# Kernel optimization log

Measured on AMD Instinct MI355X. Metric: run time of the kernel, lower is better.

## Reference

```python
import jax, jax.numpy as jnp
import numpy as np

N, E, G = 20000, 320000, 64
H, NF, EF, L, Z = 280, 5, 4, 3, 64
BN_EPS = 1e-5


def _bn(x, g, b):
    # BatchNorm1d in training mode: batch stats over dim 0, biased variance
    m = x.mean(0)
    v = x.var(0)
    return g * (x - m) * jax.lax.rsqrt(v + BN_EPS) + b


def _mlp(x, W1, b1, g1, be1, W2, b2, g2, be2):
    h = jax.nn.relu(_bn(x @ W1 + b1, g1, be1))
    return jax.nn.relu(_bn(h @ W2 + b2, g2, be2))


def setup_inputs() -> dict:
    key = jax.random.key(0)
    ks = jax.random.split(key, 24)
    s = 0.05
    inp = {
        "x": jax.random.normal(ks[0], (N, NF), jnp.float32),
        "edge_attr": jax.random.normal(ks[1], (E, EF), jnp.float32),
        "edge_index": jax.random.randint(ks[2], (2, E), 0, N),
        "batch": jnp.sort(jax.random.randint(ks[3], (N,), 0, G)),
        # input layer
        "Wi": jax.random.normal(ks[4], (NF, H), jnp.float32) * s,
        "bi": jnp.zeros((H,), jnp.float32),
        # message MLP (stacked over L layers): in = 2H+EF
        "Wm1": jax.random.normal(ks[5], (L, 2 * H + EF, H), jnp.float32) * s,
        "bm1": jnp.zeros((L, H), jnp.float32),
        "g1": jnp.ones((L, H), jnp.float32),
        "be1": jnp.zeros((L, H), jnp.float32),
        "Wm2": jax.random.normal(ks[6], (L, H, H), jnp.float32) * s,
        "bm2": jnp.zeros((L, H), jnp.float32),
        "g2": jnp.ones((L, H), jnp.float32),
        "be2": jnp.zeros((L, H), jnp.float32),
        # update MLP: in = 2H
        "Wu1": jax.random.normal(ks[7], (L, 2 * H, H), jnp.float32) * s,
        "bu1": jnp.zeros((L, H), jnp.float32),
        "g3": jnp.ones((L, H), jnp.float32),
        "be3": jnp.zeros((L, H), jnp.float32),
        "Wu2": jax.random.normal(ks[8], (L, H, H), jnp.float32) * s,
        "bu2": jnp.zeros((L, H), jnp.float32),
        "g4": jnp.ones((L, H), jnp.float32),
        "be4": jnp.zeros((L, H), jnp.float32),
        # mu head
        "Wmu": jax.random.normal(ks[9], (H, Z), jnp.float32) * s,
        "bmu": jnp.zeros((Z,), jnp.float32),
    }
    return inp


def reference(x, edge_attr, Wi, bi, Wm1, bm1, g1, be1, Wm2, bm2, g2, be2,
              Wu1, bu1, g3, be3, Wu2, bu2, g4, be4, Wmu, bmu,
              edge_index, batch):
    src, dst = edge_index[0], edge_index[1]
    h = x @ Wi + bi  # [N, H]
    for l in range(L):
        # message: cat(h_i=h[dst], h_j=h[src], edge_attr) -> MLP -> [E, H]
        msg_in = jnp.concatenate([h[dst], h[src], edge_attr], axis=-1)
        msg = _mlp(msg_in, Wm1[l], bm1[l], g1[l], be1[l], Wm2[l], bm2[l], g2[l], be2[l])
        # aggregate: scatter-add into target nodes
        agg = jax.ops.segment_sum(msg, dst, num_segments=N)
        # update: cat(h, agg) -> MLP; residual in GNNEncoder
        upd = _mlp(jnp.concatenate([h, agg], axis=-1),
                   Wu1[l], bu1[l], g3[l], be3[l], Wu2[l], bu2[l], g4[l], be4[l])
        h = h + upd
    # global mean pool over graphs
    sums = jax.ops.segment_sum(h, batch, num_segments=G)
    cnt = jax.ops.segment_sum(jnp.ones((h.shape[0],), h.dtype), batch, num_segments=G)
    pooled = sums / jnp.maximum(cnt, 1.0)[:, None]
    return pooled @ Wmu + bmu  # [G, Z]
```

## Files before the change

### kernel.cpp

```cpp
#include <hip/hip_runtime.h>
#include <hip/hip_bf16.h>

#define NN 20000
#define EE 320000
#define GG 64
#define HH 280
#define NFF 5
#define EFF 4
#define LL 3
#define ZZ 64
#define BN_EPS 1e-5f

typedef __hip_bfloat16 bf;
typedef unsigned short ush;
typedef __attribute__((ext_vector_type(8))) short v8s;
typedef __attribute__((ext_vector_type(4))) float v4f;

__device__ __forceinline__ float us2f(ush u) {
  return __uint_as_float(((unsigned)u) << 16);
}
__device__ __forceinline__ ush f2us(float v) {
  bf b = __float2bfloat16(v);
  return *reinterpret_cast<ush*>(&b);
}
__device__ __forceinline__ int clampi(int v, int hi) {
  return v < 0 ? 0 : (v >= hi ? hi - 1 : v);
}

__global__ void probe_k(const void* __restrict__ x, int* __restrict__ flag) {
  __shared__ int sh[256];
  int tid = threadIdx.x;
  int cnt = 0;
  for (int i = tid; i < 2048; i += 256) {
    ush w = ((const ush*)x)[i];
    unsigned e = (w >> 7) & 0xFF;
    if (w != 0 && (e < 87 || e > 167)) cnt++;
  }
  sh[tid] = cnt;
  __syncthreads();
  for (int o = 128; o > 0; o >>= 1) {
    if (tid < o) sh[tid] += sh[tid + o];
    __syncthreads();
  }
  if (tid == 0) *flag = (sh[0] > 64) ? 1 : 0;
}

__global__ void convert_k(const void* __restrict__ src, float* __restrict__ dst,
                          int n, const int* __restrict__ flag) {
  int i = blockIdx.x * 256 + threadIdx.x;
  if (i < n) {
    if (*flag)
      dst[i] = ((const float*)src)[i];
    else
      dst[i] = us2f(((const ush*)src)[i]);
  }
}

__global__ void wt_ab_k(const float* __restrict__ W, ush* __restrict__ O) {
  int i = blockIdx.x * 256 + threadIdx.x;
  if (i >= 3 * 576 * 288) return;
  int l = i / 165888, r = i % 165888;
  int n = r / 288, k = r % 288;
  float v = 0.f;
  if (n < 560 && k < 280)
    v = (n < 280) ? W[(size_t)l * 157920 + (size_t)k * 280 + n]
                  : W[(size_t)l * 157920 + (size_t)(280 + k) * 280 + (n - 280)];
  O[i] = f2us(v);
}
__global__ void wt_sq_k(const float* __restrict__ W, ush* __restrict__ O) {
  int i = blockIdx.x * 256 + threadIdx.x;
  if (i >= 3 * 320 * 288) return;
  int l = i / 92160, r = i % 92160;
  int n = r / 288, k = r % 288;
  float v = (n < 280 && k < 280) ? W[(size_t)l * 78400 + (size_t)k * 280 + n] : 0.f;
  O[i] = f2us(v);
}
__global__ void wt_u1_k(const float* __restrict__ W, ush* __restrict__ O) {
  int i = blockIdx.x * 256 + threadIdx.x;
  if (i >= 3 * 320 * 576) return;
  int l = i / 184320, r = i % 184320;
  int n = r / 576, k = r % 576;
  float v = (n < 280 && k < 560) ? W[(size_t)l * 156800 + (size_t)k * 280 + n] : 0.f;
  O[i] = f2us(v);
}

struct MG {
  const ush* A;
  const ush* Bt;
  const float* bias;
  void* C;
  float* stats;
  int M, K, Nn, lda, ldb, ldc;
};

template <int CB, int ST>
__global__ __launch_bounds__(256) void mgemm_k(MG g) {
  __shared__ ush As[64][40];
  __shared__ ush Bs[64][40];
  __shared__ float red[16][64];
  int t = threadIdx.x;
  int n0 = blockIdx.x * 64, m0 = blockIdx.y * 64;
  int lane = t & 63, wv = t >> 6;
  int lrow = lane & 15, quad = lane >> 4;
  int ar = t >> 2;
  int ac = (t & 3) << 3;
  v4f acc[4];
#pragma unroll
  for (int j = 0; j < 4; ++j) acc[j] = (v4f){0.f, 0.f, 0.f, 0.f};

  const ush* Ap = g.A + (size_t)(m0 + ar) * g.lda + ac;
  const ush* Bp = g.Bt + (size_t)(n0 + ar) * g.ldb + ac;
  bool av = (m0 + ar) < g.M;
  uint4 zz = {0, 0, 0, 0};

  int nkt = g.K >> 5;
  uint4 a0 = av ? *(const uint4*)Ap : zz;
  uint4 b0 = *(const uint4*)Bp;

  for (int kt = 0; kt < nkt; ++kt) {
    __syncthreads();
    *(uint4*)&As[ar][ac] = a0;
    *(uint4*)&Bs[ar][ac] = b0;
    __syncthreads();
    if (kt + 1 < nkt) {
      int kn = (kt + 1) << 5;
      a0 = av ? *(const uint4*)(Ap + kn) : zz;
      b0 = *(const uint4*)(Bp + kn);
    }
    v8s af = *(const v8s*)&As[(wv << 4) + lrow][quad << 3];
    v8s bq[4];
#pragma unroll
    for (int ci = 0; ci < 4; ++ci)
      bq[ci] = *(const v8s*)&Bs[(ci << 4) + lrow][quad << 3];
#pragma unroll
    for (int ci = 0; ci < 4; ++ci)
      acc[ci] = __builtin_amdgcn_mfma_f32_16x16x32_bf16(af, bq[ci], acc[ci],
                                                        0, 0, 0);
  }

  float bj[4];
#pragma unroll
  for (int ci = 0; ci < 4; ++ci) {
    int gn = n0 + (ci << 4) + lrow;
    bj[ci] = (g.bias && gn < g.Nn) ? g.bias[gn] : 0.f;
  }
#pragma unroll
  for (int ci = 0; ci < 4; ++ci)
#pragma unroll
    for (int r = 0; r < 4; ++r) {
      int gm = m0 + (wv << 4) + (quad << 2) + r;
      int gn = n0 + (ci << 4) + lrow;
      float v = acc[ci][r] + bj[ci];
      bool ok = (gm < g.M) && (gn < g.Nn);
      if (ok) {
        size_t idx = (size_t)gm * g.ldc + gn;
        if (CB)
          ((ush*)g.C)[idx] = f2us(v);
        else
          ((float*)g.C)[idx] = v;
      }
      acc[ci][r] = ok ? v : 0.f;
    }
  if (ST) {
    int rowg = (wv << 2) | quad;
#pragma unroll
    for (int ci = 0; ci < 4; ++ci) {
      float s = acc[ci][0] + acc[ci][1] + acc[ci][2] + acc[ci][3];
      red[rowg][(ci << 4) | lrow] = s;
    }
    __syncthreads();
    if (t < 64) {
      float s = 0.f;
#pragma unroll
      for (int r = 0; r < 16; ++r) s += red[r][t];
      int gn = n0 + t;
      if (gn < g.Nn) atomicAdd(&g.stats[gn], s);
    }
    __syncthreads();
#pragma unroll
    for (int ci = 0; ci < 4; ++ci) {
      float s = acc[ci][0] * acc[ci][0] + acc[ci][1] * acc[ci][1] +
                acc[ci][2] * acc[ci][2] + acc[ci][3] * acc[ci][3];
      red[rowg][(ci << 4) | lrow] = s;
    }
    __syncthreads();
    if (t < 64) {
      float s = 0.f;
#pragma unroll
      for (int r = 0; r < 16; ++r) s += red[r][t];
      int gn = n0 + t;
      if (gn < g.Nn) atomicAdd(&g.stats[HH + gn], s);
    }
  }
}

__global__ __launch_bounds__(256) void gemm_small_k(
    const float* __restrict__ A, const float* __restrict__ B,
    const float* __restrict__ bias, void* __restrict__ C,
    const int* __restrict__ flag, int M, int K, int Nn, int lda, int ldb,
    int ldc, int outmode) {
  __shared__ alignas(16) float As[16][68];
  __shared__ alignas(16) float Bsm[16][68];
  int tid = threadIdx.x;
  int n0 = blockIdx.x * 64, m0 = blockIdx.y * 64;
  int tx = tid & 15, ty = tid >> 4;
  int am = tid >> 2, akq = (tid & 3) << 2;
  int bk = tid >> 4, bn = (tid & 15) << 2;
  float acc[4][4] = {};
  int gmA = m0 + am;
  int nkt = (K + 15) >> 4;
  for (int kt = 0; kt < nkt; ++kt) {
    int k0 = kt << 4;
#pragma unroll
    for (int i = 0; i < 4; ++i) {
      int gk = k0 + akq + i;
      As[akq + i][am] = (gmA < M && gk < K) ? A[(size_t)gmA * lda + gk] : 0.f;
    }
    {
      int gk = k0 + bk;
      bool kin = gk < K;
#pragma unroll
      for (int j = 0; j < 4; ++j) {
        int gn = n0 + bn + j;
        Bsm[bk][bn + j] = (kin && gn < Nn) ? B[(size_t)gk * ldb + gn] : 0.f;
      }
    }
    __syncthreads();
#pragma unroll
    for (int kk = 0; kk < 16; ++kk) {
      float4 a4 = *(const float4*)&As[kk][ty << 2];
      float4 b4 = *(const float4*)&Bsm[kk][tx << 2];
      float av[4] = {a4.x, a4.y, a4.z, a4.w};
      float bv[4] = {b4.x, b4.y, b4.z, b4.w};
#pragma unroll
      for (int i = 0; i < 4; ++i)
#pragma unroll
        for (int j = 0; j < 4; ++j) acc[i][j] = fmaf(av[i], bv[j], acc[i][j]);
    }
    __syncthreads();
  }
  int ofl = outmode ? *flag : -1;
#pragma unroll
  for (int i = 0; i < 4; ++i) {
    int gm = m0 + (ty << 2) + i;
    if (gm < M) {
#pragma unroll
      for (int j = 0; j < 4; ++j) {
        int gn = n0 + (tx << 2) + j;
        if (gn < Nn) {
          float v = acc[i][j] + (bias ? bias[gn] : 0.f);
          size_t idx = (size_t)gm * ldc + gn;
          if (outmode == 0)
            ((float*)C)[idx] = v;
          else if (ofl)
            ((float*)C)[idx] = v;
          else
            ((ush*)C)[idx] = f2us(v);
        }
      }
    }
  }
}

__global__ __launch_bounds__(256) void edge_stats_k(
    const int* __restrict__ eids, const int* __restrict__ dst,
    const int* __restrict__ src, const float* __restrict__ ea,
    const ush* __restrict__ Pq, const float* __restrict__ W1c,
    const float* __restrict__ b1, float* __restrict__ stats) {
  __shared__ int dstl[256], srcl[256];
  __shared__ float4 eal[256];
  __shared__ float w1cs[4 * HH];
  __shared__ float b1s[HH];
  int tid = threadIdx.x;
  int e0 = blockIdx.x * 256;
  {
    int e = clampi(eids[e0 + tid], EE);
    dstl[tid] = clampi(dst[e], NN);
    srcl[tid] = clampi(src[e], NN);
    eal[tid] = *(const float4*)(ea + (size_t)e * 4);
  }
  for (int i = tid; i < 4 * HH; i += 256) w1cs[i] = W1c[i];
  for (int i = tid; i < HH; i += 256) b1s[i] = b1[i];
  __syncthreads();
  int c0 = tid, c1 = tid + 256;
  bool has1 = c1 < HH;
  float s0 = 0.f, q0 = 0.f, s1 = 0.f, q1 = 0.f;
  for (int e = 0; e < 256; ++e) {
    int d = dstl[e], sn = srcl[e];
    float4 ev = eal[e];
    {
      float raw = us2f(Pq[(size_t)d * 576 + c0]) + us2f(Pq[(size_t)sn * 576 + 280 + c0]);
      float r = ev.x * w1cs[c0] + ev.y * w1cs[HH + c0] +
                ev.z * w1cs[2 * HH + c0] + ev.w * w1cs[3 * HH + c0];
      float tv = raw + r + b1s[c0];
      s0 += tv; q0 += tv * tv;
    }
    if (has1) {
      float raw = us2f(Pq[(size_t)d * 576 + c1]) + us2f(Pq[(size_t)sn * 576 + 280 + c1]);
      float r = ev.x * w1cs[c1] + ev.y * w1cs[HH + c1] +
                ev.z * w1cs[2 * HH + c1] + ev.w * w1cs[3 * HH + c1];
      float tv = raw + r + b1s[c1];
      s1 += tv; q1 += tv * tv;
    }
  }
  atomicAdd(&stats[c0], s0);
  atomicAdd(&stats[HH + c0], q0);
  if (has1) {
    atomicAdd(&stats[c1], s1);
    atomicAdd(&stats[HH + c1], q1);
  }
}

__global__ void bn_finalize_k(const float* __restrict__ stats, float cnt,
                              const float* __restrict__ gw,
                              const float* __restrict__ bw,
                              const float* __restrict__ extra,
                              float* __restrict__ scale,
                              float* __restrict__ shift) {
  int c = threadIdx.x;
  if (c < HH) {
    float m = stats[c] / cnt;
    float v = stats[HH + c] / cnt - m * m;
    v = v < 0.f ? 0.f : v;
    float r = rsqrtf(v + BN_EPS);
    float sc = gw[c] * r;
    float sh = bw[c] - sc * m + (extra ? sc * extra[c] : 0.f);
    scale[c] = sc;
    shift[c] = sh;
  }
}

__global__ void hist_k(const int* __restrict__ dst, int* __restrict__ counts) {
  int e = blockIdx.x * 256 + threadIdx.x;
  if (e < EE) atomicAdd(&counts[clampi(dst[e], NN)], 1);
}

__global__ __launch_bounds__(1024) void scan_k(const int* __restrict__ counts,
                                               int* __restrict__ offs, int n) {
  __shared__ int buf[1024];
  __shared__ int running;
  int tid = threadIdx.x;
  if (tid == 0) running = 0;
  __syncthreads();
  for (int base = 0; base < n; base += 1024) {
    int v = (base + tid < n) ? counts[base + tid] : 0;
    buf[tid] = v;
    __syncthreads();
    for (int off = 1; off < 1024; off <<= 1) {
      int t = (tid >= off) ? buf[tid - off] : 0;
      __syncthreads();
      buf[tid] += t;
      __syncthreads();
    }
    int incl = buf[tid];
    if (base + tid < n) offs[base + tid] = running + incl - v;
    __syncthreads();
    if (tid == 1023) running += incl;
    __syncthreads();
  }
  if (tid == 0) offs[n] = running;
}

__global__ void fill_k(const int* __restrict__ dst, const int* __restrict__ offs,
                       int* __restrict__ cursor, int* __restrict__ eids) {
  int e = blockIdx.x * 256 + threadIdx.x;
  if (e < EE) {
    int n = clampi(dst[e], NN);
    int pos = atomicAdd(&cursor[n], 1);
    int idx = offs[n] + pos;
    if (idx >= 0 && idx < EE) eids[idx] = e;
  }
}

__global__ __launch_bounds__(256) void build_t1_k(
    const int* __restrict__ eids, const int* __restrict__ dst,
    const int* __restrict__ src, const float* __restrict__ ea,
    const ush* __restrict__ Pq, const float* __restrict__ W1c,
    const float* __restrict__ sc, const float* __restrict__ sh,
    ush* __restrict__ T1, int cb) {
  __shared__ float scs[HH], shs[HH], w1[4 * HH];
  int t = threadIdx.x;
  for (int i = t; i < HH; i += 256) { scs[i] = sc[i]; shs[i] = sh[i]; }
  for (int i = t; i < 4 * HH; i += 256) w1[i] = W1c[i];
  __syncthreads();
  int base = blockIdx.x * 32;
  int c2 = t + 256;
  bool h2 = c2 < HH;
  for (int i = 0; i < 32; ++i) {
    int r = cb + base + i;
    int e = clampi(eids[r], EE);
    int d = clampi(dst[e], NN), s = clampi(src[e], NN);
    float4 ev = *(const float4*)(ea + (size_t)e * 4);
    size_t pd = (size_t)d * 576, ps = (size_t)s * 576 + 280;
    size_t orow = (size_t)(base + i) * 288;
    {
      int c = t;
      float v = us2f(Pq[pd + c]) + us2f(Pq[ps + c]) + ev.x * w1[c] +
                ev.y * w1[HH + c] + ev.z * w1[2 * HH + c] + ev.w * w1[3 * HH + c];
      v = fmaf(scs[c], v, shs[c]);
      T1[orow + c] = f2us(v > 0.f ? v : 0.f);
    }
    if (h2) {
      int c = c2;
      float v = us2f(Pq[pd + c]) + us2f(Pq[ps + c]) + ev.x * w1[c] +
                ev.y * w1[HH + c] + ev.z * w1[2 * HH + c] + ev.w * w1[3 * HH + c];
      v = fmaf(scs[c], v, shs[c]);
      T1[orow + c] = f2us(v > 0.f ? v : 0.f);
    }
  }
}

__global__ __launch_bounds__(256) void aggregate_k(
    const int* __restrict__ offs, const ush* __restrict__ tmp2,
    const float* __restrict__ scale, const float* __restrict__ shift,
    float* __restrict__ agg, int e0, int e1) {
  int n = blockIdx.x;
  int rs = offs[n], re = offs[n + 1];
  if (rs < e0) rs = e0;
  if (re > e1) re = e1;
  if (rs >= re) return;
  int t = threadIdx.x;
  int c2 = t + 256;
  bool h2 = c2 < HH;
  float a0 = 0.f, a1 = 0.f;
  float sc0 = scale[t], sh0 = shift[t];
  float sc1 = h2 ? scale[c2] : 0.f, sh1 = h2 ? shift[c2] : 0.f;
  for (int r = rs; r < re; ++r) {
    const ush* row = tmp2 + (size_t)(r - e0) * HH;
    float v0 = fmaf(sc0, us2f(row[t]), sh0);
    a0 += v0 > 0.f ? v0 : 0.f;
    if (h2) {
      float v1 = fmaf(sc1, us2f(row[c2]), sh1);
      a1 += v1 > 0.f ? v1 : 0.f;
    }
  }
  agg[(size_t)n * HH + t] += a0;
  if (h2) agg[(size_t)n * HH + c2] += a1;
}

__global__ void hb_k(const float* __restrict__ h, ush* __restrict__ hcat) {
  int i = blockIdx.x * 256 + threadIdx.x;
  if (i < NN * HH) {
    int n = i / HH, c = i % HH;
    hcat[(size_t)n * 576 + c] = f2us(h[i]);
  }
}
__global__ void agg2hcat_k(const float* __restrict__ agg, ush* __restrict__ hcat) {
  int i = blockIdx.x * 256 + threadIdx.x;
  if (i < NN * HH) {
    int n = i / HH, c = i % HH;
    hcat[(size_t)n * 576 + 280 + c] = f2us(agg[i]);
  }
}
__global__ void u2a_k(const float* __restrict__ u1, const float* __restrict__ sc,
                      const float* __restrict__ sh, ush* __restrict__ u2A) {
  int i = blockIdx.x * 256 + threadIdx.x;
  if (i < NN * HH) {
    int n = i / HH, c = i % HH;
    float v = fmaf(sc[c], u1[i], sh[c]);
    u2A[(size_t)n * 288 + c] = f2us(v > 0.f ? v : 0.f);
  }
}
__global__ void residual_k(float* __restrict__ h, const float* __restrict__ u2,
                           const float* __restrict__ scale,
                           const float* __restrict__ shift) {
  int i = blockIdx.x * 256 + threadIdx.x;
  if (i < NN * HH) {
    int c = i % HH;
    float v = fmaf(scale[c], u2[i], shift[c]);
    h[i] += v > 0.f ? v : 0.f;
  }
}

__device__ __forceinline__ int lowerb(const int* a, int n, int key) {
  int lo = 0, hi = n;
  while (lo < hi) {
    int mid = (lo + hi) >> 1;
    if (a[mid] < key) lo = mid + 1; else hi = mid;
  }
  return lo;
}

__global__ __launch_bounds__(256) void pool_k(const float* __restrict__ h,
                                              const int* __restrict__ batch,
                                              float* __restrict__ pooled) {
  __shared__ float red[4][56];
  int gid = blockIdx.x, cc = blockIdx.y;
  int start = lowerb(batch, NN, gid);
  int end = lowerb(batch, NN, gid + 1);
  int cnt = end - start;
  float inv = 1.f / (float)(cnt > 1 ? cnt : 1);
  int grp = threadIdx.x >> 6, ci = threadIdx.x & 63;
  if (ci < 56) {
    int col = cc * 56 + ci;
    float s = 0.f;
    for (int n = start + grp; n < end; n += 4) s += h[(size_t)n * HH + col];
    red[grp][ci] = s;
  }
  __syncthreads();
  if (threadIdx.x < 56) {
    float s = red[0][threadIdx.x] + red[1][threadIdx.x] +
              red[2][threadIdx.x] + red[3][threadIdx.x];
    pooled[(size_t)gid * HH + cc * 56 + threadIdx.x] = s * inv;
  }
}

extern "C" void kernel_launch(void* const* d_in, const int* in_sizes, int n_in,
                              void* d_out, int out_size, void* d_ws,
                              size_t ws_size, hipStream_t stream) {
  const int* eidx = (const int*)d_in[2];
  const int* batch = (const int*)d_in[3];
  const int* srcp = eidx;
  const int* dstp = eidx + EE;
  size_t NH = (size_t)NN * HH;

  float* w0 = (float*)d_ws;
  size_t off = 0;
  auto alloc = [&](size_t n) {
    float* p = w0 + off;
    off += (n + 3) & ~(size_t)3;
    return p;
  };
  int* flag = (int*)alloc(4);
  float* cx = alloc(100000);
  float* cea = alloc(1280000);
  float* cWi = alloc(1400);
  float* cbi = alloc(280);
  float* cWm1 = alloc(473760);
  float* cbm1 = alloc(840);
  float* cg1 = alloc(840);
  float* cbe1 = alloc(840);
  float* cWm2 = alloc(235200);
  float* cbm2 = alloc(840);
  float* cg2 = alloc(840);
  float* cbe2 = alloc(840);
  float* cWu1 = alloc(470400);
  float* cbu1 = alloc(840);
  float* cg3 = alloc(840);
  float* cbe3 = alloc(840);
  float* cWu2 = alloc(235200);
  float* cbu2 = alloc(840);
  float* cg4 = alloc(840);
  float* cbe4 = alloc(840);
  float* cWmu = alloc(17920);
  float* cbmu = alloc(64);
  ush* W1ab = (ush*)alloc(248832);
  ush* W2t = (ush*)alloc(138240);
  ush* WU1t = (ush*)alloc(276480);
  ush* WU2t = (ush*)alloc(138240);
  float* h = alloc(NH);
  ush* hcat = (ush*)alloc(5824512);
  ush* u2A = hcat;
  float* pqr = alloc(5824512);
  ush* Pq = (ush*)pqr;
  float* u1f = pqr;
  float* agg = alloc(NH);
  float* pooled = alloc((size_t)GG * HH);
  float* stats = alloc(8 * HH);
  float* ss = alloc(8 * HH);
  int* counts = (int*)alloc(NN);
  int* offs = (int*)alloc(NN + 1);
  int* cursor = (int*)alloc(NN);
  int* eids = (int*)alloc(EE);
  size_t baseB = off * 4;

  int EC = 6400, T2 = 6400;
  {
    const int ecs[5] = {64000, 64000, 32000, 12800, 6400};
    const int t2s[5] = {EE, 64000, 32000, 12800, 6400};
    for (int i = 0; i < 5; ++i) {
      size_t need = baseB + (size_t)ecs[i] * 288 * 2 + (size_t)t2s[i] * 280 * 2 + 64;
      if (need <= ws_size) { EC = ecs[i]; T2 = t2s[i]; break; }
    }
  }
  ush* T1c = (ush*)(w0 + off);
  ush* tmp2 = T1c + (size_t)EC * 288;
  bool stored = (T2 == EE);
  int nch = EE / EC;

  probe_k<<<1, 256, 0, stream>>>(d_in[0], flag);
  struct Cv { const void* s; float* d; int n; };
  const Cv cv[22] = {
      {d_in[0], cx, NN * NFF},     {d_in[1], cea, EE * EFF},
      {d_in[4], cWi, NFF * HH},    {d_in[5], cbi, HH},
      {d_in[6], cWm1, LL * (2 * HH + EFF) * HH}, {d_in[7], cbm1, LL * HH},
      {d_in[8], cg1, LL * HH},     {d_in[9], cbe1, LL * HH},
      {d_in[10], cWm2, LL * HH * HH}, {d_in[11], cbm2, LL * HH},
      {d_in[12], cg2, LL * HH},    {d_in[13], cbe2, LL * HH},
      {d_in[14], cWu1, LL * 2 * HH * HH}, {d_in[15], cbu1, LL * HH},
      {d_in[16], cg3, LL * HH},    {d_in[17], cbe3, LL * HH},
      {d_in[18], cWu2, LL * HH * HH}, {d_in[19], cbu2, LL * HH},
      {d_in[20], cg4, LL * HH},    {d_in[21], cbe4, LL * HH},
      {d_in[22], cWmu, HH * ZZ},   {d_in[23], cbmu, ZZ}};
  for (int i = 0; i < 22; ++i)
    convert_k<<<(cv[i].n + 255) / 256, 256, 0, stream>>>(cv[i].s, cv[i].d, cv[i].n, flag);

  wt_ab_k<<<(3 * 576 * 288 + 255) / 256, 256, 0, stream>>>(cWm1, W1ab);
  wt_sq_k<<<(3 * 320 * 288 + 255) / 256, 256, 0, stream>>>(cWm2, W2t);
  wt_u1_k<<<(3 * 320 * 576 + 255) / 256, 256, 0, stream>>>(cWu1, WU1t);
  wt_sq_k<<<(3 * 320 * 288 + 255) / 256, 256, 0, stream>>>(cWu2, WU2t);

  gemm_small_k<<<dim3(5, 313), 256, 0, stream>>>(cx, cWi, cbi, h, nullptr, NN,
                                                 NFF, HH, NFF, HH, HH, 0);
  hipMemsetAsync(counts, 0, NN * sizeof(int), stream);
  hipMemsetAsync(cursor, 0, NN * sizeof(int), stream);
  hist_k<<<(EE + 255) / 256, 256, 0, stream>>>(dstp, counts);
  scan_k<<<1, 1024, 0, stream>>>(counts, offs, NN);
  fill_k<<<(EE + 255) / 256, 256, 0, stream>>>(dstp, offs, cursor, eids);

  int elemGrid = (int)((NH + 255) / 256);
  for (int l = 0; l < LL; ++l) {
    ush* Wab = W1ab + (size_t)l * 576 * 288;
    ush* W2l = W2t + (size_t)l * 320 * 288;
    ush* WU1l = WU1t + (size_t)l * 320 * 576;
    ush* WU2l = WU2t + (size_t)l * 320 * 288;
    const float* W1c = cWm1 + (size_t)l * 157920 + (size_t)560 * 280;
    float* st1 = stats; float* st2 = stats + 560;
    float* st3 = stats + 1120; float* st4 = stats + 1680;
    float* ss1 = ss; float* ss2 = ss + 560;
    float* ss3 = ss + 1120; float* ss4 = ss + 1680;
    hipMemsetAsync(stats, 0, 8 * HH * sizeof(float), stream);

    hb_k<<<elemGrid, 256, 0, stream>>>(h, hcat);
    {
      MG g = {hcat, Wab, nullptr, Pq, nullptr, NN, 288, 560, 576, 288, 576};
      mgemm_k<1, 0><<<dim3(9, 313), 256, 0, stream>>>(g);
    }
    edge_stats_k<<<EE / 256, 256, 0, stream>>>(eids, dstp, srcp, cea, Pq, W1c,
                                               cbm1 + l * HH, st1);
    bn_finalize_k<<<1, 320, 0, stream>>>(st1, (float)EE, cg1 + l * HH,
                                         cbe1 + l * HH, cbm1 + l * HH, ss1, ss1 + HH);
    for (int c = 0; c < nch; ++c) {
      int cb = c * EC;
      build_t1_k<<<EC / 32, 256, 0, stream>>>(eids, dstp, srcp, cea, Pq, W1c,
                                              ss1, ss1 + HH, T1c, cb);
      MG g = {T1c, W2l, cbm2 + l * HH,
              stored ? (void*)(tmp2 + (size_t)cb * HH) : (void*)tmp2, st2,
              EC, 288, HH, 288, 288, HH};
      mgemm_k<1, 1><<<dim3(5, EC / 64), 256, 0, stream>>>(g);
    }
    bn_finalize_k<<<1, 320, 0, stream>>>(st2, (float)EE, cg2 + l * HH,
                                         cbe2 + l * HH, nullptr, ss2, ss2 + HH);
    hipMemsetAsync(agg, 0, NH * sizeof(float), stream);
    if (stored) {
      aggregate_k<<<NN, 256, 0, stream>>>(offs, tmp2, ss2, ss2 + HH, agg, 0, EE);
    } else {
      for (int c = 0; c < nch; ++c) {
        int cb = c * EC;
        build_t1_k<<<EC / 32, 256, 0, stream>>>(eids, dstp, srcp, cea, Pq, W1c,
                                                ss1, ss1 + HH, T1c, cb);
        MG g = {T1c, W2l, cbm2 + l * HH, (void*)tmp2, nullptr,
                EC, 288, HH, 288, 288, HH};
        mgemm_k<1, 0><<<dim3(5, EC / 64), 256, 0, stream>>>(g);
        aggregate_k<<<NN, 256, 0, stream>>>(offs, tmp2, ss2, ss2 + HH, agg, cb, cb + EC);
      }
    }
    agg2hcat_k<<<elemGrid, 256, 0, stream>>>(agg, hcat);
    {
      MG g = {hcat, WU1l, cbu1 + l * HH, u1f, st3, NN, 576, HH, 576, 576, HH};
      mgemm_k<0, 1><<<dim3(5, 313), 256, 0, stream>>>(g);
    }
    bn_finalize_k<<<1, 320, 0, stream>>>(st3, (float)NN, cg3 + l * HH,
                                         cbe3 + l * HH, nullptr, ss3, ss3 + HH);
    u2a_k<<<elemGrid, 256, 0, stream>>>(u1f, ss3, ss3 + HH, u2A);
    {
      MG g = {u2A, WU2l, cbu2 + l * HH, agg, st4, NN, 288, HH, 288, 288, HH};
      mgemm_k<0, 1><<<dim3(5, 313), 256, 0, stream>>>(g);
    }
    bn_finalize_k<<<1, 320, 0, stream>>>(st4, (float)NN, cg4 + l * HH,
                                         cbe4 + l * HH, nullptr, ss4, ss4 + HH);
    residual_k<<<elemGrid, 256, 0, stream>>>(h, agg, ss4, ss4 + HH);
  }

  pool_k<<<dim3(GG, 5), 256, 0, stream>>>(h, batch, pooled);
  gemm_small_k<<<dim3(1, 1), 256, 0, stream>>>(pooled, cWmu, cbmu, d_out, flag,
                                               GG, HH, ZZ, HH, ZZ, ZZ, 1);
}
```

Measured before the change: 4.591 ms.

## Restructure MFMA GEMM to stage full-K B tile in LDS and stream A via registers

```diff
diff --git a/kernel.cpp b/kernel.cpp
--- a/kernel.cpp
+++ b/kernel.cpp
@@ -95,47 +95,61 @@
 
 template <int CB, int ST>
 __global__ __launch_bounds__(256) void mgemm_k(MG g) {
-  __shared__ ush As[64][40];
-  __shared__ ush Bs[64][40];
-  __shared__ float red[16][64];
+  __shared__ ush Bs[64][296];
+  auto red = (float(*)[64])Bs;
   int t = threadIdx.x;
-  int n0 = blockIdx.x * 64, m0 = blockIdx.y * 64;
+  int n0 = blockIdx.x * 64, m0 = blockIdx.y * 128;
   int lane = t & 63, wv = t >> 6;
   int lrow = lane & 15, quad = lane >> 4;
-  int ar = t >> 2;
-  int ac = (t & 3) << 3;
-  v4f acc[4];
-#pragma unroll
-  for (int j = 0; j < 4; ++j) acc[j] = (v4f){0.f, 0.f, 0.f, 0.f};
-
-  const ush* Ap = g.A + (size_t)(m0 + ar) * g.lda + ac;
-  const ush* Bp = g.Bt + (size_t)(n0 + ar) * g.ldb + ac;
-  bool av = (m0 + ar) < g.M;
+  int br = t >> 2;
+  int bc = (t & 3) * 72;
+  v4f acc[2][4];
+#pragma unroll
+  for (int gi = 0; gi < 2; ++gi)
+#pragma unroll
+    for (int ci = 0; ci < 4; ++ci) acc[gi][ci] = (v4f){0.f, 0.f, 0.f, 0.f};
+
+  const ush* Arow[2];
+  bool av[2];
+#pragma unroll
+  for (int gi = 0; gi < 2; ++gi) {
+    int gm = m0 + (wv << 5) + (gi << 4) + lrow;
+    av[gi] = gm < g.M;
+    Arow[gi] = g.A + (size_t)gm * g.lda + (quad << 3);
+  }
+  const ush* Brow = g.Bt + (size_t)(n0 + br) * g.ldb + bc;
   uint4 zz = {0, 0, 0, 0};
 
-  int nkt = g.K >> 5;
-  uint4 a0 = av ? *(const uint4*)Ap : zz;
-  uint4 b0 = *(const uint4*)Bp;
-
-  for (int kt = 0; kt < nkt; ++kt) {
-    __syncthreads();
-    *(uint4*)&As[ar][ac] = a0;
-    *(uint4*)&Bs[ar][ac] = b0;
-    __syncthreads();
-    if (kt + 1 < nkt) {
-      int kn = (kt + 1) << 5;
-      a0 = av ? *(const uint4*)(Ap + kn) : zz;
-      b0 = *(const uint4*)(Bp + kn);
-    }
-    v8s af = *(const v8s*)&As[(wv << 4) + lrow][quad << 3];
-    v8s bq[4];
-#pragma unroll
-    for (int ci = 0; ci < 4; ++ci)
-      bq[ci] = *(const v8s*)&Bs[(ci << 4) + lrow][quad << 3];
-#pragma unroll
-    for (int ci = 0; ci < 4; ++ci)
-      acc[ci] = __builtin_amdgcn_mfma_f32_16x16x32_bf16(af, bq[ci], acc[ci],
-                                                        0, 0, 0);
+  int ntile = g.K / 288;
+  for (int tile = 0; tile < ntile; ++tile) {
+    int k0 = tile * 288;
+    uint4 aR[2][9];
+#pragma unroll
+    for (int kt = 0; kt < 9; ++kt)
+#pragma unroll
+      for (int gi = 0; gi < 2; ++gi)
+        aR[gi][kt] =
+            av[gi] ? *(const uint4*)(Arow[gi] + k0 + (kt << 5)) : zz;
+    if (tile) __syncthreads();
+#pragma unroll
+    for (int i = 0; i < 9; ++i)
+      *(uint4*)&Bs[br][bc + (i << 3)] = *(const uint4*)(Brow + k0 + (i << 3));
+    __syncthreads();
+#pragma unroll
+    for (int kt = 0; kt < 9; ++kt) {
+      v8s bq[4];
+#pragma unroll
+      for (int ci = 0; ci < 4; ++ci)
+        bq[ci] = *(const v8s*)&Bs[(ci << 4) + lrow][(kt << 5) + (quad << 3)];
+#pragma unroll
+      for (int gi = 0; gi < 2; ++gi) {
+        v8s af = *(v8s*)&aR[gi][kt];
+#pragma unroll
+        for (int ci = 0; ci < 4; ++ci)
+          acc[gi][ci] = __builtin_amdgcn_mfma_f32_16x16x32_bf16(
+              af, bq[ci], acc[gi][ci], 0, 0, 0);
+      }
+    }
   }
 
   float bj[4];
@@ -145,27 +159,34 @@
     bj[ci] = (g.bias && gn < g.Nn) ? g.bias[gn] : 0.f;
   }
 #pragma unroll
-  for (int ci = 0; ci < 4; ++ci)
-#pragma unroll
-    for (int r = 0; r < 4; ++r) {
-      int gm = m0 + (wv << 4) + (quad << 2) + r;
-      int gn = n0 + (ci << 4) + lrow;
-      float v = acc[ci][r] + bj[ci];
-      bool ok = (gm < g.M) && (gn < g.Nn);
-      if (ok) {
-        size_t idx = (size_t)gm * g.ldc + gn;
-        if (CB)
-          ((ush*)g.C)[idx] = f2us(v);
-        else
-          ((float*)g.C)[idx] = v;
+  for (int gi = 0; gi < 2; ++gi)
+#pragma unroll
+    for (int ci = 0; ci < 4; ++ci)
+#pragma unroll
+      for (int r = 0; r < 4; ++r) {
+        int gm = m0 + (wv << 5) + (gi << 4) + (quad << 2) + r;
+        int gn = n0 + (ci << 4) + lrow;
+        float v = acc[gi][ci][r] + bj[ci];
+        bool ok = (gm < g.M) && (gn < g.Nn);
+        if (ok) {
+          size_t idx = (size_t)gm * g.ldc + gn;
+          if (CB)
+            ((ush*)g.C)[idx] = f2us(v);
+          else
+            ((float*)g.C)[idx] = v;
+        }
+        acc[gi][ci][r] = ok ? v : 0.f;
       }
-      acc[ci][r] = ok ? v : 0.f;
-    }
   if (ST) {
     int rowg = (wv << 2) | quad;
+    __syncthreads();
 #pragma unroll
     for (int ci = 0; ci < 4; ++ci) {
-      float s = acc[ci][0] + acc[ci][1] + acc[ci][2] + acc[ci][3];
+      float s = 0.f;
+#pragma unroll
+      for (int gi = 0; gi < 2; ++gi)
+#pragma unroll
+        for (int r = 0; r < 4; ++r) s += acc[gi][ci][r];
       red[rowg][(ci << 4) | lrow] = s;
     }
     __syncthreads();
@@ -179,8 +200,11 @@
     __syncthreads();
 #pragma unroll
     for (int ci = 0; ci < 4; ++ci) {
-      float s = acc[ci][0] * acc[ci][0] + acc[ci][1] * acc[ci][1] +
-                acc[ci][2] * acc[ci][2] + acc[ci][3] * acc[ci][3];
+      float s = 0.f;
+#pragma unroll
+      for (int gi = 0; gi < 2; ++gi)
+#pragma unroll
+        for (int r = 0; r < 4; ++r) s += acc[gi][ci][r] * acc[gi][ci][r];
       red[rowg][(ci << 4) | lrow] = s;
     }
     __syncthreads();
@@ -624,7 +648,7 @@
     hb_k<<<elemGrid, 256, 0, stream>>>(h, hcat);
     {
       MG g = {hcat, Wab, nullptr, Pq, nullptr, NN, 288, 560, 576, 288, 576};
-      mgemm_k<1, 0><<<dim3(9, 313), 256, 0, stream>>>(g);
+      mgemm_k<1, 0><<<dim3(9, 157), 256, 0, stream>>>(g);
     }
     edge_stats_k<<<EE / 256, 256, 0, stream>>>(eids, dstp, srcp, cea, Pq, W1c,
                                                cbm1 + l * HH, st1);
@@ -637,7 +661,7 @@
       MG g = {T1c, W2l, cbm2 + l * HH,
               stored ? (void*)(tmp2 + (size_t)cb * HH) : (void*)tmp2, st2,
               EC, 288, HH, 288, 288, HH};
-      mgemm_k<1, 1><<<dim3(5, EC / 64), 256, 0, stream>>>(g);
+      mgemm_k<1, 1><<<dim3(5, EC / 128), 256, 0, stream>>>(g);
     }
     bn_finalize_k<<<1, 320, 0, stream>>>(st2, (float)EE, cg2 + l * HH,
                                          cbe2 + l * HH, nullptr, ss2, ss2 + HH);
@@ -651,21 +675,22 @@
                                                 ss1, ss1 + HH, T1c, cb);
         MG g = {T1c, W2l, cbm2 + l * HH, (void*)tmp2, nullptr,
                 EC, 288, HH, 288, 288, HH};
-        mgemm_k<1, 0><<<dim3(5, EC / 64), 256, 0, stream>>>(g);
+        mgemm_k<1, 0><<<dim3(5, EC / 128), 256, 0, stream>>>(g);
         aggregate_k<<<NN, 256, 0, stream>>>(offs, tmp2, ss2, ss2 + HH, agg, cb, cb + EC);
       }
     }
     agg2hcat_k<<<elemGrid, 256, 0, stream>>>(agg, hcat);
     {
       MG g = {hcat, WU1l, cbu1 + l * HH, u1f, st3, NN, 576, HH, 576, 576, HH};
-      mgemm_k<0, 1><<<dim3(5, 313), 256, 0, stream>>>(g);
+      mgemm_k<0, 1><<<dim3(5, 157), 256, 0, stream>>>(g);
     }
     bn_finalize_k<<<1, 320, 0, stream>>>(st3, (float)NN, cg3 + l * HH,
                                          cbe3 + l * HH, nullptr, ss3, ss3 + HH);
     u2a_k<<<elemGrid, 256, 0, stream>>>(u1f, ss3, ss3 + HH, u2A);
     {
-      MG g = {u2A, WU2l, cbu2 + l * HH, agg, st4, NN, 288, HH, 288, 288, HH};
-      mgemm_k<0, 1><<<dim3(5, 313), 256, 0, stream>>>(g);
+      MG g = {u2A, WU2t + (size_t)l * 320 * 288, cbu2 + l * HH, agg, st4,
+              NN, 288, HH, 288, 288, HH};
+      mgemm_k<0, 1><<<dim3(5, 157), 256, 0, stream>>>(g);
     }
     bn_finalize_k<<<1, 320, 0, stream>>>(st4, (float)NN, cg4 + l * HH,
                                          cbe4 + l * HH, nullptr, ss4, ss4 + HH);
```

Measured after the change: 4.275 ms. 1.07x faster.
